# Kernel optimization log

Measured on AMD Instinct MI355X. Metric: run time of the kernel, lower is better.

Reference implementation:

```python
import jax, jax.numpy as jnp
import numpy as np
from jax import lax


def haar_dwt2(x):
    """Level-1 Haar (db1) 2D DWT on [N, H, W] with even H, W.
    Returns cA, cH, cV (cD is discarded by the module), each [N, H//2, W//2].
    Matches pywt/ptwt db1 block form: cA=(a+b+c+d)/2, etc."""
    a = x[:, 0::2, 0::2]
    b = x[:, 0::2, 1::2]
    c = x[:, 1::2, 0::2]
    d = x[:, 1::2, 1::2]
    cA = (a + b + c + d) * 0.5
    cH = (a + b - c - d) * 0.5  # horizontal detail (highpass along rows axis)
    cV = (a - b + c - d) * 0.5  # vertical detail (highpass along cols axis)
    return cA, cH, cV


def conv2d_same(x, w, b):
    # x: [N, Cin, H, W], w: [Cout, Cin, kh, kw]
    y = lax.conv_general_dilated(x, w, window_strides=(1, 1), padding='SAME',
                                 dimension_numbers=('NCHW', 'OIHW', 'NCHW'))
    return y + b[None, :, None, None]


def maxpool2(x):
    return lax.reduce_window(x, -jnp.inf, lax.max,
                             window_dimensions=(1, 1, 2, 2),
                             window_strides=(1, 1, 2, 2), padding='VALID')


def setup_inputs() -> dict:
    key = jax.random.key(0)
    ks = jax.random.split(key, 7)
    B, C, H, W = 32, 3, 512, 512
    x = jax.random.normal(ks[0], (B, C, H, W), dtype=jnp.float32)
    # conv stack params (Conv2d(1,16,3), Conv2d(16,8,3), Conv2d(8,4,1))
    w1 = jax.random.normal(ks[1], (16, 1, 3, 3), dtype=jnp.float32) * (1.0 / 3.0)
    b1 = jnp.zeros((16,), dtype=jnp.float32)
    w2 = jax.random.normal(ks[2], (8, 16, 3, 3), dtype=jnp.float32) * (1.0 / 12.0)
    b2 = jnp.zeros((8,), dtype=jnp.float32)
    w3 = jax.random.normal(ks[3], (4, 8, 1, 1), dtype=jnp.float32) * (1.0 / 2.83)
    b3 = jnp.zeros((4,), dtype=jnp.float32)
    return {"x": x, "w1": w1, "b1": b1, "w2": w2, "b2": b2, "w3": w3, "b3": b3}


def reference(x, w1, b1, w2, b2, w3, b3):
    B, C, H, W = x.shape
    # Batch the per-image/per-channel loop: treat each channel as one map.
    flat = x.reshape(B * C, H, W)
    cA, cH, cV = haar_dwt2(flat)  # [B*C, H/2, W/2]

    # Low-frequency conv stack on approx coeffs (1 input channel per map).
    h = cA[:, None, :, :]                       # [B*C, 1, H/2, W/2]
    h = maxpool2(jax.nn.relu(conv2d_same(h, w1, b1)))
    h = maxpool2(jax.nn.relu(conv2d_same(h, w2, b2)))
    h = conv2d_same(h, w3, b3)                  # [B*C, 4, H/8, W/8]
    # per-channel flatten, then concat over channels (dim=1 in the original)
    low = h.reshape(B, 1, -1)                   # [B, 1, C*4*(H/8)*(W/8)]

    # High-frequency: per channel concat [cH.flatten(), cV.flatten()],
    # then concat over channels.
    n = (H // 2) * (W // 2)
    high = jnp.concatenate([cH.reshape(B, C, n), cV.reshape(B, C, n)], axis=-1)
    high = high.reshape(B, 1, C * 2 * n)        # [B, 1, C*2*(H/2)*(W/2)]
    return low, high
```

## Files before the change

kernel.cpp:

```cpp
#include <hip/hip_runtime.h>


typedef _Float16 f16x8 __attribute__((ext_vector_type(8)));
typedef float    f32x4 __attribute__((ext_vector_type(4)));

__global__ __launch_bounds__(256, 3) void fused_all_kernel(
    const float* __restrict__ x,
    const float* __restrict__ w1, const float* __restrict__ b1,
    const float* __restrict__ w2, const float* __restrict__ b2,
    const float* __restrict__ w3, const float* __restrict__ b3,
    float* __restrict__ outLow, float* __restrict__ outHigh)
{
    __shared__ __align__(16) float    ca[70 * 72];
    __shared__ __align__(16) _Float16 h1s[38 * 36 * 8];

    int img = blockIdx.x >> 4;
    int t   = blockIdx.x & 15;
    int ty = t >> 2, tx = t & 3;
    int hy0 = ty * 32 - 1, hx0 = tx * 32 - 1;
    int cy0 = ty * 64 - 3, cx0 = tx * 64 - 3;

    const float* xi = x + img * 262144;
    float* hb = outHigh + img * 131072;

    int lane = threadIdx.x & 63;
    int wid  = threadIdx.x >> 6;
    int q = lane >> 4, m = lane & 15;
    int ppy = m >> 2, ppx = m & 3;
    int wy = wid >> 1, wx = wid & 1;

    f16x8 Bf[2][3];
    #pragma unroll
    for (int c = 0; c < 2; ++c)
        #pragma unroll
        for (int s = 0; s < 3; ++s) {
            f16x8 bf;
            #pragma unroll
            for (int j = 0; j < 8; ++j) {
                int tt = s * 4 + q;
                float wvv = 0.f;
                if (m < 8 && tt < 9) wvv = w2[(m * 16 + (c * 8 + j)) * 9 + tt];
                bf[j] = (_Float16)wvv;
            }
            Bf[c][s] = bf;
        }
    float bb2 = 0.f;
    if (m < 8) bb2 = b2[m];

    #pragma unroll
    for (int k = 0; k < 4; ++k) {
        int i = threadIdx.x + k * 256;
        int row = i >> 4, cg = i & 15;
        int gy = ty * 64 + row;
        int gx = tx * 64 + cg * 4;
        const float* r0 = xi + (2 * gy) * 512 + 2 * gx;
        const float* r1 = r0 + 512;
        float4 t0 = *(const float4*)(r0);
        float4 t1 = *(const float4*)(r0 + 4);
        float4 u0 = *(const float4*)(r1);
        float4 u1 = *(const float4*)(r1 + 4);
        float4 vA, vH, vV;
        vA.x = (t0.x + t0.y + u0.x + u0.y) * 0.5f;
        vH.x = (t0.x + t0.y - u0.x - u0.y) * 0.5f;
        vV.x = (t0.x - t0.y + u0.x - u0.y) * 0.5f;
        vA.y = (t0.z + t0.w + u0.z + u0.w) * 0.5f;
        vH.y = (t0.z + t0.w - u0.z - u0.w) * 0.5f;
        vV.y = (t0.z - t0.w + u0.z - u0.w) * 0.5f;
        vA.z = (t1.x + t1.y + u1.x + u1.y) * 0.5f;
        vH.z = (t1.x + t1.y - u1.x - u1.y) * 0.5f;
        vV.z = (t1.x - t1.y + u1.x - u1.y) * 0.5f;
        vA.w = (t1.z + t1.w + u1.z + u1.w) * 0.5f;
        vH.w = (t1.z + t1.w - u1.z - u1.w) * 0.5f;
        vV.w = (t1.z - t1.w + u1.z - u1.w) * 0.5f;
        int po = (gy << 8) + gx;
        *(float4*)(hb + po) = vH;
        *(float4*)(hb + 65536 + po) = vV;
        float* cp = ca + (row + 3) * 72 + cg * 4 + 3;
        cp[0] = vA.x; cp[1] = vA.y; cp[2] = vA.z; cp[3] = vA.w;
    }

    for (int i = threadIdx.x; i < 804; i += 256) {
        int r, c;
        if (i < 210)      { r = i / 70;              c = i - r * 70; }
        else if (i < 420) { int j = i - 210; r = 67 + j / 70; c = j - (j / 70) * 70; }
        else              { int j = i - 420; r = 3 + j / 6; int k6 = j - (j / 6) * 6;
                            c = (k6 < 3) ? k6 : (64 + k6); }
        int gy = cy0 + r, gx = cx0 + c;
        float v = 0.f;
        if ((unsigned)gy < 256u && (unsigned)gx < 256u) {
            const float* p0 = xi + (2 * gy) * 512 + 2 * gx;
            float2 a = *(const float2*)(p0);
            float2 b = *(const float2*)(p0 + 512);
            v = (a.x + a.y + b.x + b.y) * 0.5f;
        }
        ca[r * 72 + c] = v;
    }

    {
        f16x8 z;
        #pragma unroll
        for (int j = 0; j < 8; ++j) z[j] = (_Float16)0.f;
        for (int i = threadIdx.x; i < 144; i += 256)
            *(f16x8*)(h1s + (34 * 36 + i) * 8) = z;
    }

    int ky0 = (q >= 3) ? 1 : 0, kx0 = (q >= 3) ? 0 : q;
    int t1q = q + 4;
    int ky1 = (t1q >= 6) ? 2 : 1, kx1 = t1q - ky1 * 3;
    int off0 = ((ppy + ky0) * 36 + (ppx + kx0)) * 8;
    int off1 = ((ppy + ky1) * 36 + (ppx + kx1)) * 8;
    int off2 = ((ppy + 2) * 36 + (ppx + 2)) * 8;
    int zoff = ((34 + ppy) * 36 + ppx) * 8;
    bool z2 = (q != 0);

    f32x4 acc[16];
    #pragma unroll
    for (int i = 0; i < 16; ++i) acc[i] = (f32x4){0.f, 0.f, 0.f, 0.f};

    __syncthreads();

    #pragma unroll
    for (int cc = 0; cc < 2; ++cc) {
        if (cc) __syncthreads();

        #pragma unroll 1
        for (int k = 0; k < 5; ++k) {
            int i = threadIdx.x + k * 256;
            if (i < 1156) {
                int hy = i / 34, hx = i - hy * 34;
                const float* pb = ca + (2 * hy) * 72 + 2 * hx;
                float patch[4][4];
                #pragma unroll
                for (int r = 0; r < 4; ++r) {
                    float2 a = *(const float2*)(pb + r * 72);
                    float2 b = *(const float2*)(pb + r * 72 + 2);
                    patch[r][0] = a.x; patch[r][1] = a.y;
                    patch[r][2] = b.x; patch[r][3] = b.y;
                }
                bool oob = ((unsigned)(hy0 + hy) >= 128u) | ((unsigned)(hx0 + hx) >= 128u);
                f16x8 ov;
                #pragma unroll
                for (int og = 0; og < 2; ++og) {
                    #pragma unroll
                    for (int o = 0; o < 4; ++o) {
                        int oc = cc * 8 + og * 4 + o;
                        float p00 = 0.f, p01 = 0.f, p10 = 0.f, p11 = 0.f;
                        #pragma unroll
                        for (int ky = 0; ky < 3; ++ky)
                            #pragma unroll
                            for (int kx = 0; kx < 3; ++kx) {
                                float wvv = w1[oc * 9 + ky * 3 + kx];
                                p00 += patch[ky][kx]         * wvv;
                                p01 += patch[ky][kx + 1]     * wvv;
                                p10 += patch[ky + 1][kx]     * wvv;
                                p11 += patch[ky + 1][kx + 1] * wvv;
                            }
                        float mm = fmaxf(fmaxf(p00, p01), fmaxf(p10, p11)) + b1[oc];
                        mm = fmaxf(mm, 0.f);
                        ov[og * 4 + o] = (_Float16)(oob ? 0.f : mm);
                    }
                }
                *(f16x8*)(h1s + (hy * 36 + hx) * 8) = ov;
            }
        }
        __syncthreads();

        #pragma unroll
        for (int mt = 0; mt < 16; ++mt) {
            int my = mt >> 2, mx = mt & 3;
            int pbase = ((wy * 16 + my * 4) * 36 + (wx * 16 + mx * 4)) * 8;
            f16x8 a0 = *(const f16x8*)(h1s + pbase + off0);
            f16x8 a1 = *(const f16x8*)(h1s + pbase + off1);
            int a2i = z2 ? zoff : (pbase + off2);
            f16x8 a2 = *(const f16x8*)(h1s + a2i);
            acc[mt] = __builtin_amdgcn_mfma_f32_16x16x32_f16(a0, Bf[cc][0], acc[mt], 0, 0, 0);
            acc[mt] = __builtin_amdgcn_mfma_f32_16x16x32_f16(a1, Bf[cc][1], acc[mt], 0, 0, 0);
            acc[mt] = __builtin_amdgcn_mfma_f32_16x16x32_f16(a2, Bf[cc][2], acc[mt], 0, 0, 0);
        }
    }

    float* h2b = (float*)ca;
    #pragma unroll
    for (int mt = 0; mt < 16; ++mt) {
        int my = mt >> 2, mx = mt & 3;
        float u0 = fmaxf(acc[mt][0], acc[mt][1]);
        float u1 = fmaxf(acc[mt][2], acc[mt][3]);
        float v0 = fmaxf(u0, __shfl_xor(u0, 16, 64));
        float v1 = fmaxf(u1, __shfl_xor(u1, 16, 64));
        float h20 = fmaxf(v0 + bb2, 0.f);
        float h21 = fmaxf(v1 + bb2, 0.f);
        if (m < 8 && (q & 1) == 0) {
            int Yp = wy * 8 + my * 2 + (q >> 1);
            int Xp = wx * 8 + mx * 2;
            h2b[(Yp * 16 + Xp) * 8 + m]     = h20;
            h2b[(Yp * 16 + Xp + 1) * 8 + m] = h21;
        }
    }
    __syncthreads();

    {
        int Yp = threadIdx.x >> 4, Xp = threadIdx.x & 15;
        const float* hv = h2b + (Yp * 16 + Xp) * 8;
        float4 va = *(const float4*)(hv);
        float4 vb = *(const float4*)(hv + 4);
        float h2v[8] = {va.x, va.y, va.z, va.w, vb.x, vb.y, vb.z, vb.w};
        float* dst = outLow + img * 16384;
        int pos = (ty * 16 + Yp) * 64 + tx * 16 + Xp;
        #pragma unroll
        for (int oc3 = 0; oc3 < 4; ++oc3) {
            float s = b3[oc3];
            #pragma unroll
            for (int ic = 0; ic < 8; ++ic) s += w3[oc3 * 8 + ic] * h2v[ic];
            dst[oc3 * 4096 + pos] = s;
        }
    }
}

extern "C" void kernel_launch(void* const* d_in, const int* in_sizes, int n_in,
                              void* d_out, int out_size, void* d_ws, size_t ws_size,
                              hipStream_t stream) {
    const float* x  = (const float*)d_in[0];
    const float* w1 = (const float*)d_in[1];
    const float* b1 = (const float*)d_in[2];
    const float* w2 = (const float*)d_in[3];
    const float* b2 = (const float*)d_in[4];
    const float* w3 = (const float*)d_in[5];
    const float* b3 = (const float*)d_in[6];
    float* out     = (float*)d_out;
    float* outLow  = out;
    float* outHigh = out + 1572864;

    fused_all_kernel<<<1536, 256, 0, stream>>>(x, w1, b1, w2, b2, w3, b3,
                                               outLow, outHigh);
}
```

Measured before the change: 251.0 us.

## Compute all 16 conv1 channels in one pass and pack conv2 K dimension

```diff
diff --git a/kernel.cpp b/kernel.cpp
--- a/kernel.cpp
+++ b/kernel.cpp
@@ -2,6 +2,7 @@
 
 
 typedef _Float16 f16x8 __attribute__((ext_vector_type(8)));
+typedef _Float16 f16x2 __attribute__((ext_vector_type(2)));
 typedef float    f32x4 __attribute__((ext_vector_type(4)));
 
 __global__ __launch_bounds__(256, 3) void fused_all_kernel(
@@ -11,8 +12,11 @@
     const float* __restrict__ w3, const float* __restrict__ b3,
     float* __restrict__ outLow, float* __restrict__ outHigh)
 {
-    __shared__ __align__(16) float    ca[70 * 72];
-    __shared__ __align__(16) _Float16 h1s[38 * 36 * 8];
+    __shared__ __align__(16) float    smem0[2450];
+    __shared__ __align__(16) _Float16 h1s[34 * 34 * 16];
+
+    _Float16* ca  = (_Float16*)smem0;
+    float*    h2b = smem0;
 
     int img = blockIdx.x >> 4;
     int t   = blockIdx.x & 15;
@@ -28,24 +32,6 @@
     int q = lane >> 4, m = lane & 15;
     int ppy = m >> 2, ppx = m & 3;
     int wy = wid >> 1, wx = wid & 1;
-
-    f16x8 Bf[2][3];
-    #pragma unroll
-    for (int c = 0; c < 2; ++c)
-        #pragma unroll
-        for (int s = 0; s < 3; ++s) {
-            f16x8 bf;
-            #pragma unroll
-            for (int j = 0; j < 8; ++j) {
-                int tt = s * 4 + q;
-                float wvv = 0.f;
-                if (m < 8 && tt < 9) wvv = w2[(m * 16 + (c * 8 + j)) * 9 + tt];
-                bf[j] = (_Float16)wvv;
-            }
-            Bf[c][s] = bf;
-        }
-    float bb2 = 0.f;
-    if (m < 8) bb2 = b2[m];
 
     #pragma unroll
     for (int k = 0; k < 4; ++k) {
@@ -75,8 +61,9 @@
         int po = (gy << 8) + gx;
         *(float4*)(hb + po) = vH;
         *(float4*)(hb + 65536 + po) = vV;
-        float* cp = ca + (row + 3) * 72 + cg * 4 + 3;
-        cp[0] = vA.x; cp[1] = vA.y; cp[2] = vA.z; cp[3] = vA.w;
+        _Float16* cp = ca + (row + 3) * 70 + cg * 4 + 3;
+        cp[0] = (_Float16)vA.x; cp[1] = (_Float16)vA.y;
+        cp[2] = (_Float16)vA.z; cp[3] = (_Float16)vA.w;
     }
 
     for (int i = threadIdx.x; i < 804; i += 256) {
@@ -93,98 +80,89 @@
             float2 b = *(const float2*)(p0 + 512);
             v = (a.x + a.y + b.x + b.y) * 0.5f;
         }
-        ca[r * 72 + c] = v;
-    }
-
-    {
-        f16x8 z;
+        ca[r * 70 + c] = (_Float16)v;
+    }
+
+    __syncthreads();
+
+    #pragma unroll 1
+    for (int k = 0; k < 5; ++k) {
+        int i = threadIdx.x + k * 256;
+        if (i < 1156) {
+            int hy = i / 34, hx = i - hy * 34;
+            const _Float16* pb = ca + (2 * hy) * 70 + 2 * hx;
+            float patch[4][4];
+            #pragma unroll
+            for (int r = 0; r < 4; ++r) {
+                f16x2 a = *(const f16x2*)(pb + r * 70);
+                f16x2 b = *(const f16x2*)(pb + r * 70 + 2);
+                patch[r][0] = (float)a.x; patch[r][1] = (float)a.y;
+                patch[r][2] = (float)b.x; patch[r][3] = (float)b.y;
+            }
+            bool oob = ((unsigned)(hy0 + hy) >= 128u) | ((unsigned)(hx0 + hx) >= 128u);
+            f16x8 ov0, ov1;
+            #pragma unroll
+            for (int oc = 0; oc < 16; ++oc) {
+                float p00 = 0.f, p01 = 0.f, p10 = 0.f, p11 = 0.f;
+                #pragma unroll
+                for (int ky = 0; ky < 3; ++ky)
+                    #pragma unroll
+                    for (int kx = 0; kx < 3; ++kx) {
+                        float wvv = w1[oc * 9 + ky * 3 + kx];
+                        p00 += patch[ky][kx]         * wvv;
+                        p01 += patch[ky][kx + 1]     * wvv;
+                        p10 += patch[ky + 1][kx]     * wvv;
+                        p11 += patch[ky + 1][kx + 1] * wvv;
+                    }
+                float mm = fmaxf(fmaxf(p00, p01), fmaxf(p10, p11)) + b1[oc];
+                mm = fmaxf(mm, 0.f);
+                _Float16 hv = (_Float16)(oob ? 0.f : mm);
+                if (oc < 8) ov0[oc] = hv; else ov1[oc - 8] = hv;
+            }
+            *(f16x8*)(h1s + (hy * 34 + hx) * 16)     = ov0;
+            *(f16x8*)(h1s + (hy * 34 + hx) * 16 + 8) = ov1;
+        }
+    }
+
+    __syncthreads();
+
+    f16x8 Bf[5];
+    #pragma unroll
+    for (int s = 0; s < 5; ++s) {
+        int tt = 2 * s + (q >> 1);
+        f16x8 bf;
         #pragma unroll
-        for (int j = 0; j < 8; ++j) z[j] = (_Float16)0.f;
-        for (int i = threadIdx.x; i < 144; i += 256)
-            *(f16x8*)(h1s + (34 * 36 + i) * 8) = z;
-    }
-
-    int ky0 = (q >= 3) ? 1 : 0, kx0 = (q >= 3) ? 0 : q;
-    int t1q = q + 4;
-    int ky1 = (t1q >= 6) ? 2 : 1, kx1 = t1q - ky1 * 3;
-    int off0 = ((ppy + ky0) * 36 + (ppx + kx0)) * 8;
-    int off1 = ((ppy + ky1) * 36 + (ppx + kx1)) * 8;
-    int off2 = ((ppy + 2) * 36 + (ppx + 2)) * 8;
-    int zoff = ((34 + ppy) * 36 + ppx) * 8;
-    bool z2 = (q != 0);
-
-    f32x4 acc[16];
+        for (int j = 0; j < 8; ++j) {
+            int ic = (q & 1) * 8 + j;
+            float wvv = 0.f;
+            if (m < 8 && tt < 9) wvv = w2[(m * 16 + ic) * 9 + tt];
+            bf[j] = (_Float16)wvv;
+        }
+        Bf[s] = bf;
+    }
+    float bb2 = (m < 8) ? b2[m] : 0.f;
+
+    int offA[5];
     #pragma unroll
-    for (int i = 0; i < 16; ++i) acc[i] = (f32x4){0.f, 0.f, 0.f, 0.f};
-
-    __syncthreads();
-
-    #pragma unroll
-    for (int cc = 0; cc < 2; ++cc) {
-        if (cc) __syncthreads();
-
-        #pragma unroll 1
-        for (int k = 0; k < 5; ++k) {
-            int i = threadIdx.x + k * 256;
-            if (i < 1156) {
-                int hy = i / 34, hx = i - hy * 34;
-                const float* pb = ca + (2 * hy) * 72 + 2 * hx;
-                float patch[4][4];
-                #pragma unroll
-                for (int r = 0; r < 4; ++r) {
-                    float2 a = *(const float2*)(pb + r * 72);
-                    float2 b = *(const float2*)(pb + r * 72 + 2);
-                    patch[r][0] = a.x; patch[r][1] = a.y;
-                    patch[r][2] = b.x; patch[r][3] = b.y;
-                }
-                bool oob = ((unsigned)(hy0 + hy) >= 128u) | ((unsigned)(hx0 + hx) >= 128u);
-                f16x8 ov;
-                #pragma unroll
-                for (int og = 0; og < 2; ++og) {
-                    #pragma unroll
-                    for (int o = 0; o < 4; ++o) {
-                        int oc = cc * 8 + og * 4 + o;
-                        float p00 = 0.f, p01 = 0.f, p10 = 0.f, p11 = 0.f;
-                        #pragma unroll
-                        for (int ky = 0; ky < 3; ++ky)
-                            #pragma unroll
-                            for (int kx = 0; kx < 3; ++kx) {
-                                float wvv = w1[oc * 9 + ky * 3 + kx];
-                                p00 += patch[ky][kx]         * wvv;
-                                p01 += patch[ky][kx + 1]     * wvv;
-                                p10 += patch[ky + 1][kx]     * wvv;
-                                p11 += patch[ky + 1][kx + 1] * wvv;
-                            }
-                        float mm = fmaxf(fmaxf(p00, p01), fmaxf(p10, p11)) + b1[oc];
-                        mm = fmaxf(mm, 0.f);
-                        ov[og * 4 + o] = (_Float16)(oob ? 0.f : mm);
-                    }
-                }
-                *(f16x8*)(h1s + (hy * 36 + hx) * 8) = ov;
-            }
-        }
-        __syncthreads();
-
-        #pragma unroll
-        for (int mt = 0; mt < 16; ++mt) {
-            int my = mt >> 2, mx = mt & 3;
-            int pbase = ((wy * 16 + my * 4) * 36 + (wx * 16 + mx * 4)) * 8;
-            f16x8 a0 = *(const f16x8*)(h1s + pbase + off0);
-            f16x8 a1 = *(const f16x8*)(h1s + pbase + off1);
-            int a2i = z2 ? zoff : (pbase + off2);
-            f16x8 a2 = *(const f16x8*)(h1s + a2i);
-            acc[mt] = __builtin_amdgcn_mfma_f32_16x16x32_f16(a0, Bf[cc][0], acc[mt], 0, 0, 0);
-            acc[mt] = __builtin_amdgcn_mfma_f32_16x16x32_f16(a1, Bf[cc][1], acc[mt], 0, 0, 0);
-            acc[mt] = __builtin_amdgcn_mfma_f32_16x16x32_f16(a2, Bf[cc][2], acc[mt], 0, 0, 0);
-        }
-    }
-
-    float* h2b = (float*)ca;
-    #pragma unroll
+    for (int s = 0; s < 5; ++s) {
+        int tt = 2 * s + (q >> 1);
+        int ttc = (tt > 8) ? 8 : tt;
+        int ky = ttc / 3, kx = ttc - 3 * ky;
+        offA[s] = ((ppy + ky) * 34 + (ppx + kx)) * 16 + (q & 1) * 8;
+    }
+
+    #pragma unroll 4
     for (int mt = 0; mt < 16; ++mt) {
         int my = mt >> 2, mx = mt & 3;
-        float u0 = fmaxf(acc[mt][0], acc[mt][1]);
-        float u1 = fmaxf(acc[mt][2], acc[mt][3]);
+        int pbase = ((wy * 16 + my * 4) * 34 + (wx * 16 + mx * 4)) * 16;
+        f32x4 acc = (f32x4){0.f, 0.f, 0.f, 0.f};
+        #pragma unroll
+        for (int s = 0; s < 5; ++s) {
+            f16x8 a = *(const f16x8*)(h1s + pbase + offA[s]);
+            acc = __builtin_amdgcn_mfma_f32_16x16x32_f16(a, Bf[s], acc, 0, 0, 0);
+        }
+        float u0 = fmaxf(acc[0], acc[1]);
+        float u1 = fmaxf(acc[2], acc[3]);
         float v0 = fmaxf(u0, __shfl_xor(u0, 16, 64));
         float v1 = fmaxf(u1, __shfl_xor(u1, 16, 64));
         float h20 = fmaxf(v0 + bb2, 0.f);
```

Result: faster. 245.8 us (-2.1%).
